# Kernel tuning notes

Hardware: AMD Instinct MI355X
Metric: run time of the kernel (lower is better)

Reference implementation:

```python
import jax, jax.numpy as jnp
import numpy as np

D = 768          # TGLU_hidden_dim == input_hidden_dim
E = 8            # num_experts
TOP_K = 2        # top_experts
N_ENT = 32       # num_entity
B = 16           # batch (mentions)
L = 128          # max_seq_len
EPS = 1e-5


def setup_inputs() -> dict:
    key = jax.random.key(0)
    ks = jax.random.split(key, 16)
    s = 0.02
    return {
        "entity_text_cls": jax.random.normal(ks[0], (N_ENT, D), jnp.float32),
        "entity_text_tokens": jax.random.normal(ks[1], (N_ENT, L, D), jnp.float32),
        "mention_text_cls": jax.random.normal(ks[2], (B, D), jnp.float32),
        "mention_text_tokens": jax.random.normal(ks[3], (B, L, D), jnp.float32),
        # SwitchMoE params: gate + per-expert Linear(dim -> output_dim)
        "gate_w": jax.random.normal(ks[4], (D, E), jnp.float32) * s,
        "gate_b": jnp.zeros((E,), jnp.float32),
        "exp_w": jax.random.normal(ks[5], (E, D, D), jnp.float32) * s,
        "exp_b": jnp.zeros((E, D), jnp.float32),
        # attention projections
        "wq": jax.random.normal(ks[6], (D, D), jnp.float32) * s,
        "bq": jnp.zeros((D,), jnp.float32),
        "wk": jax.random.normal(ks[7], (D, D), jnp.float32) * s,
        "bk": jnp.zeros((D,), jnp.float32),
        "wv": jax.random.normal(ks[8], (D, D), jnp.float32) * s,
        "bv": jnp.zeros((D,), jnp.float32),
        # LayerNorm params
        "ln_w": jnp.ones((D,), jnp.float32),
        "ln_b": jnp.zeros((D,), jnp.float32),
    }


def _switch_moe(x, gate_w, gate_b, exp_w, exp_b):
    # x: [n, s, D] -> [n, s, D]; top-k router, renormalized combine.
    logits = jnp.einsum("nsd,de->nse", x, gate_w) + gate_b
    probs = jax.nn.softmax(logits, axis=-1)
    vals, idx = jax.lax.top_k(probs, TOP_K)              # [n,s,k]
    vals = vals / jnp.sum(vals, axis=-1, keepdims=True)
    # combine weights over all experts (zero for unselected) -> dense mask form
    w = jnp.sum(jax.nn.one_hot(idx, E, dtype=x.dtype) * vals[..., None], axis=-2)  # [n,s,E]
    eo = jnp.einsum("nsd,edo->nseo", x, exp_w) + exp_b   # [n,s,E,D]
    return jnp.einsum("nse,nseo->nso", w, eo)


def _layernorm(x, w, b):
    mu = jnp.mean(x, axis=-1, keepdims=True)
    var = jnp.mean(jnp.square(x - mu), axis=-1, keepdims=True)
    return (x - mu) * jax.lax.rsqrt(var + EPS) * w + b


def reference(entity_text_cls, entity_text_tokens, mention_text_cls, mention_text_tokens,
              gate_w, gate_b, exp_w, exp_b, wq, bq, wk, bk, wv, bv, ln_w, ln_b):
    # prepend CLS, route through shared MoE
    ent = jnp.concatenate([entity_text_cls[:, None, :], entity_text_tokens], axis=1)   # [N,L+1,D]
    ent_moe = _switch_moe(ent, gate_w, gate_b, exp_w, exp_b)
    ent_cls_moe = ent_moe[:, 0, :]          # [N,D]
    ent_tok = ent_moe[:, 1:, :]             # [N,L,D]

    men = jnp.concatenate([mention_text_cls[:, None, :], mention_text_tokens], axis=1)  # [B,L+1,D]
    men_moe = _switch_moe(men, gate_w, gate_b, exp_w, exp_b)
    men_tok = men_moe[:, 1:, :]             # [B,L,D]

    q = jnp.einsum("nld,do->nlo", ent_tok, wq) + bq    # [N,L,D]
    k = jnp.einsum("bmd,do->bmo", men_tok, wk) + bk    # [B,L,D]
    v = jnp.einsum("bmd,do->bmo", men_tok, wv) + bv    # [B,L,D]

    # all-pairs entity x mention cross attention: [N,B,L,L]
    scores = jnp.einsum("nld,bmd->nblm", q, k) / jnp.sqrt(jnp.asarray(D, q.dtype))
    probs = jax.nn.softmax(scores, axis=-1)
    context = jnp.einsum("nblm,bmd->nbld", probs, v)   # [N,B,L,D]
    context = jnp.mean(context, axis=-2)               # [N,B,D]
    context = _layernorm(context, ln_w, ln_b)

    g2l = jnp.sum(ent_cls_moe[:, None, :] * context, axis=-1)   # [N,B]
    g2l = g2l.T                                                  # [B,N]
    g2g = mention_text_cls @ entity_text_cls.T                   # [B,N]
    return (g2l + g2g) / 2
```

## Files before the change

kernel.cpp:

```cpp
#include <hip/hip_runtime.h>
#include <math.h>

#define D 768
#define NE 8
#define NTOK 6192
#define MEN_TOK0 4128

typedef __attribute__((ext_vector_type(8))) short short8;
typedef __attribute__((ext_vector_type(4))) short short4b;
typedef __attribute__((ext_vector_type(4))) float floatx4;

__device__ __forceinline__ short f2bf(float f) {
  union { float f; unsigned u; } x; x.f = f;
  unsigned r = x.u + 0x7fffu + ((x.u >> 16) & 1u);
  return (short)(r >> 16);
}
__device__ __forceinline__ float bf2f(short s) {
  union { unsigned u; float f; } x; x.u = ((unsigned)(unsigned short)s) << 16;
  return x.f;
}

__device__ __forceinline__ void gload16(const short* g, short8* lds_base) {
  __builtin_amdgcn_global_load_lds(
      (const __attribute__((address_space(1))) unsigned int*)g,
      (__attribute__((address_space(3))) unsigned int*)lds_base,
      16, 0, 0);
}

__device__ __forceinline__ const float* token_row(int t,
    const float* __restrict__ ecls, const float* __restrict__ etok,
    const float* __restrict__ mcls, const float* __restrict__ mtok) {
  if (t < MEN_TOK0) {
    int n = t / 129, s = t - n * 129;
    return (s == 0) ? (ecls + n * D) : (etok + (size_t)(n * 128 + s - 1) * D);
  } else {
    int tm = t - MEN_TOK0;
    int b = tm / 129, s = tm - b * 129;
    return (s == 0) ? (mcls + b * D) : (mtok + (size_t)(b * 128 + s - 1) * D);
  }
}

__global__ __launch_bounds__(256) void prep_kernel(
    const float* __restrict__ ecls, const float* __restrict__ etok,
    const float* __restrict__ mcls, const float* __restrict__ mtok,
    const float* __restrict__ gate_w, const float* __restrict__ gate_b,
    const float* __restrict__ exp_w, const float* __restrict__ wq,
    const float* __restrict__ wk, const float* __restrict__ wv,
    int* __restrict__ te1, int* __restrict__ te2,
    float* __restrict__ tw1, float* __restrict__ tw2,
    short* __restrict__ Xb, short* __restrict__ expwT, short* __restrict__ wT) {
  __shared__ float tbuf[64][65];
  int bid = blockIdx.x;
  int tid = threadIdx.x;
  if (bid < 1548) {
    int t = bid * 4 + (tid >> 6);
    int lane = tid & 63;
    const float* xr = token_row(t, ecls, etok, mcls, mtok);
    float acc[NE];
#pragma unroll
    for (int e = 0; e < NE; ++e) acc[e] = 0.f;
#pragma unroll
    for (int it = 0; it < 3; ++it) {
      int d0 = lane * 4 + it * 256;
      floatx4 x = *(const floatx4*)(xr + d0);
      short4b xb;
#pragma unroll
      for (int q = 0; q < 4; ++q) {
        xb[q] = f2bf(x[q]);
        float xv = x[q];
#pragma unroll
        for (int e = 0; e < NE; ++e) acc[e] += xv * gate_w[(d0 + q) * NE + e];
      }
      *(short4b*)(Xb + (size_t)t * D + d0) = xb;
    }
#pragma unroll
    for (int e = 0; e < NE; ++e) {
#pragma unroll
      for (int off = 32; off > 0; off >>= 1) acc[e] += __shfl_down(acc[e], off);
    }
    if (lane == 0) {
      float lg[NE];
#pragma unroll
      for (int e = 0; e < NE; ++e) lg[e] = acc[e] + gate_b[e];
      int e1 = 0;
#pragma unroll
      for (int e = 1; e < NE; ++e) if (lg[e] > lg[e1]) e1 = e;
      int e2 = (e1 == 0) ? 1 : 0;
#pragma unroll
      for (int e = 0; e < NE; ++e) {
        if (e != e1 && lg[e] > lg[e2]) e2 = e;
      }
      float w1 = 1.f / (1.f + __expf(lg[e2] - lg[e1]));
      te1[t] = e1; te2[t] = e2;
      tw1[t] = w1; tw2[t] = 1.f - w1;
    }
  } else {
    int zz = bid - 1548;
    int z = zz / 144, rem = zz % 144;
    int k0 = (rem / 12) * 64, o0 = (rem % 12) * 64;
    const float* src; short* dst;
    if (z < 8) { src = exp_w + (size_t)z * D * D; dst = expwT + (size_t)z * D * D; }
    else { src = (z == 8) ? wq : (z == 9) ? wk : wv; dst = wT + (size_t)(z - 8) * D * D; }
    int tx = tid & 63, ty = tid >> 6;
#pragma unroll
    for (int i = 0; i < 16; ++i) {
      int k = i * 4 + ty;
      tbuf[k][tx] = src[(size_t)(k0 + k) * D + o0 + tx];
    }
    __syncthreads();
#pragma unroll
    for (int i = 0; i < 16; ++i) {
      int o = i * 4 + ty;
      dst[(size_t)(o0 + o) * D + k0 + tx] = f2bf(tbuf[tx][o]);
    }
  }
}

__global__ __launch_bounds__(1024) void route_kernel(
    const int* __restrict__ te1, const int* __restrict__ te2,
    int* __restrict__ lst_tok, int* __restrict__ slot1, int* __restrict__ slot2,
    int* __restrict__ cnt, int* __restrict__ basee) {
  __shared__ int hist[NE];
  __shared__ int base_s[NE];
  int tid = threadIdx.x;
  if (tid < NE) hist[tid] = 0;
  __syncthreads();
  for (int t = tid; t < NTOK; t += 1024) {
    atomicAdd(&hist[te1[t]], 1);
    atomicAdd(&hist[te2[t]], 1);
  }
  __syncthreads();
  if (tid == 0) {
    int acc = 0;
    for (int e = 0; e < NE; ++e) {
      base_s[e] = acc;
      cnt[e] = hist[e];
      basee[e] = acc;
      acc += hist[e];
    }
  }
  __syncthreads();
  if (tid < NE) hist[tid] = 0;
  __syncthreads();
  for (int t = tid; t < NTOK; t += 1024) {
    int e1 = te1[t], e2 = te2[t];
    int r1 = atomicAdd(&hist[e1], 1);
    int r2 = atomicAdd(&hist[e2], 1);
    int s1 = base_s[e1] + r1;
    int s2 = base_s[e2] + r2;
    slot1[t] = s1; slot2[t] = s2;
    lst_tok[s1] = t; lst_tok[s2] = t;
  }
}

__global__ __launch_bounds__(512, 4) void moe_kernel(
    const short* __restrict__ Xb, const short* __restrict__ expwT,
    const int* __restrict__ cnt, const int* __restrict__ basee,
    const int* __restrict__ lst_tok, short* __restrict__ EO) {
  int id = blockIdx.x;
  int e = id & 7;
  int r = id >> 3;
  int ob = r % 6;
  int tb = r / 6;
  int count = cnt[e];
  int t0 = tb * 128;
  if (t0 >= count) return;
  int o0 = ob * 128;
  int gb = basee[e];

  __shared__ short8 As[1024];
  __shared__ short8 Bs[1024];
  __shared__ int stok[128];

  int tid = threadIdx.x;
  int l = tid & 63, w = tid >> 6;
  int wr = w >> 1, wc = w & 1;

  if (tid < 128) {
    int p = t0 + tid;
    stok[tid] = lst_tok[gb + (p < count ? p : 0)];
  }
  __syncthreads();

  const short* Bg = expwT + (size_t)e * D * D;
  int srow = tid >> 2, scc = tid & 3;
  int csrc = (scc ^ ((srow >> 1) & 3)) * 8;
  const short* srcA = Xb + (size_t)stok[srow] * D + csrc;
  const short* srcB = Bg + (size_t)(o0 + srow) * D + csrc;

  floatx4 acc[2][4];
#pragma unroll
  for (int ai = 0; ai < 2; ++ai)
#pragma unroll
    for (int bj = 0; bj < 4; ++bj) acc[ai][bj] = (floatx4){0.f, 0.f, 0.f, 0.f};

  gload16(srcA, &As[w << 6]);
  gload16(srcB, &Bs[w << 6]);
  __syncthreads();

  for (int it = 0; it < 24; ++it) {
    int cur = (it & 1) << 9;
    if (it < 23) {
      int k0n = (it + 1) * 32;
      gload16(srcA + k0n, &As[(cur ^ 512) + (w << 6)]);
      gload16(srcB + k0n, &Bs[(cur ^ 512) + (w << 6)]);
    }
    int kc = l >> 4;
    short8 a[2], bb[4];
#pragma unroll
    for (int ai = 0; ai < 2; ++ai) {
      int ar = wr * 32 + ai * 16 + (l & 15);
      a[ai] = As[cur + (ar << 2) + (kc ^ ((ar >> 1) & 3))];
    }
#pragma unroll
    for (int bj = 0; bj < 4; ++bj) {
      int br = wc * 64 + bj * 16 + (l & 15);
      bb[bj] = Bs[cur + (br << 2) + (kc ^ ((br >> 1) & 3))];
    }
#pragma unroll
    for (int ai = 0; ai < 2; ++ai)
#pragma unroll
      for (int bj = 0; bj < 4; ++bj)
        acc[ai][bj] = __builtin_amdgcn_mfma_f32_16x16x32_bf16(a[ai], bb[bj], acc[ai][bj], 0, 0, 0);
    __syncthreads();
  }

#pragma unroll
  for (int ai = 0; ai < 2; ++ai) {
#pragma unroll
    for (int rr = 0; rr < 4; ++rr) {
      int rowl = wr * 32 + ai * 16 + ((l >> 4) << 2) + rr;
      int p = t0 + rowl;
      if (p < count) {
        size_t off = (size_t)(gb + p) * D;
#pragma unroll
        for (int bj = 0; bj < 4; ++bj) {
          int col = o0 + wc * 64 + bj * 16 + (l & 15);
          EO[off + col] = f2bf(acc[ai][bj][rr]);
        }
      }
    }
  }
}

__global__ __launch_bounds__(256) void combine_kernel(
    const short* __restrict__ EO,
    const int* __restrict__ te1, const int* __restrict__ te2,
    const float* __restrict__ tw1, const float* __restrict__ tw2,
    const int* __restrict__ slot1, const int* __restrict__ slot2,
    const float* __restrict__ exp_b, short* __restrict__ MOEb) {
  int idx = blockIdx.x * 256 + threadIdx.x;
  int t = idx / 96, cg = idx - t * 96;
  int c0 = cg * 8;
  int e1 = te1[t], e2 = te2[t];
  float w1 = tw1[t], w2 = tw2[t];
  short8 a = *(const short8*)(EO + (size_t)slot1[t] * D + c0);
  short8 b = *(const short8*)(EO + (size_t)slot2[t] * D + c0);
  const float* b1 = exp_b + e1 * D + c0;
  const float* b2 = exp_b + e2 * D + c0;
  short8 o;
#pragma unroll
  for (int j = 0; j < 8; ++j)
    o[j] = f2bf(w1 * (bf2f(a[j]) + b1[j]) + w2 * (bf2f(b[j]) + b2[j]));
  *(short8*)(MOEb + (size_t)t * D + c0) = o;
}

__global__ __launch_bounds__(512, 4) void qkv_kernel(
    const short* __restrict__ MOEb, const short* __restrict__ wT,
    const float* __restrict__ bq, const float* __restrict__ bk,
    const float* __restrict__ bv,
    short* __restrict__ Qb, short* __restrict__ Kb, short* __restrict__ Vb) {
  int id = blockIdx.x;
  int z, r;
  if (id < 384)      { z = 0; r = id; }
  else if (id < 576) { z = 1; r = id - 384; }
  else               { z = 2; r = id - 576; }
  int tb = r / 6, ob = r % 6;
  int o0 = ob * 128;
  int base = (z == 0) ? 0 : MEN_TOK0;
  const short* W = wT + (size_t)z * D * D;
  const float* bias = (z == 0) ? bq : (z == 1) ? bk : bv;
  int tokbase = base + (tb >> 1) * 129 + 1 + (tb & 1) * 64;
  const short* Ag = MOEb + (size_t)tokbase * D;

  __shared__ short8 As[512];
  __shared__ short8 Bs[1024];

  int tid = threadIdx.x;
  int l = tid & 63, w = tid >> 6;
  int wr = w >> 1, wc = w & 1;

  int srow = tid >> 2, scc = tid & 3;
  int csrc = (scc ^ ((srow >> 1) & 3)) * 8;
  const short* srcA = Ag + (size_t)(srow & 63) * D + csrc;
  const short* srcB = W + (size_t)(o0 + srow) * D + csrc;

  floatx4 acc[4];
#pragma unroll
  for (int bj = 0; bj < 4; ++bj) acc[bj] = (floatx4){0.f, 0.f, 0.f, 0.f};

  if (w < 4) gload16(srcA, &As[w << 6]);
  gload16(srcB, &Bs[w << 6]);
  __syncthreads();

  for (int it = 0; it < 24; ++it) {
    int curA = (it & 1) << 8;
    int curB = (it & 1) << 9;
    if (it < 23) {
      int k0n = (it + 1) * 32;
      if (w < 4) gload16(srcA + k0n, &As[(curA ^ 256) + (w << 6)]);
      gload16(srcB + k0n, &Bs[(curB ^ 512) + (w << 6)]);
    }
    int kc = l >> 4;
    int ar = wr * 16 + (l & 15);
    short8 a = As[curA + (ar << 2) + (kc ^ ((ar >> 1) & 3))];
    short8 bb[4];
#pragma unroll
    for (int bj = 0; bj < 4; ++bj) {
      int br = wc * 64 + bj * 16 + (l & 15);
      bb[bj] = Bs[curB + (br << 2) + (kc ^ ((br >> 1) & 3))];
    }
#pragma unroll
    for (int bj = 0; bj < 4; ++bj)
      acc[bj] = __builtin_amdgcn_mfma_f32_16x16x32_bf16(a, bb[bj], acc[bj], 0, 0, 0);
    __syncthreads();
  }

#pragma unroll
  for (int rr = 0; rr < 4; ++rr) {
    int rowl = wr * 16 + ((l >> 4) << 2) + rr;
    size_t rglob = (size_t)tb * 64 + rowl;
#pragma unroll
    for (int bj = 0; bj < 4; ++bj) {
      int col = o0 + wc * 64 + bj * 16 + (l & 15);
      float v = acc[bj][rr] + bias[col];
      if (z == 0)      Qb[rglob * D + col] = f2bf(v);
      else if (z == 1) Kb[rglob * D + col] = f2bf(v);
      else             Vb[rglob * D + col] = f2bf(v);
    }
  }
}

__device__ __forceinline__ float blockSum512(float v, volatile float* red, int tid) {
#pragma unroll
  for (int off = 32; off > 0; off >>= 1) v += __shfl_down(v, off);
  __syncthreads();
  if ((tid & 63) == 0) red[tid >> 6] = v;
  __syncthreads();
  float s = 0.f;
#pragma unroll
  for (int i = 0; i < 8; ++i) s += red[i];
  return s;
}

__global__ __launch_bounds__(512, 4) void attn_kernel(
    const short* __restrict__ Qb, const short* __restrict__ Kb,
    const short* __restrict__ Vb, const short* __restrict__ MOEb,
    const float* __restrict__ ecls, const float* __restrict__ mcls,
    const float* __restrict__ ln_w, const float* __restrict__ ln_b,
    float* __restrict__ out) {
  int id = blockIdx.x;
  int n = id & 31, b = id >> 5;
  __shared__ short8 Qs[1024];
  __shared__ short8 Ks[1024];
  __shared__ float pb[128];
  __shared__ float red[8];
  int tid = threadIdx.x;
  int l = tid & 63, w = tid >> 6;
  if (tid < 128) pb[tid] = 0.f;

  floatx4 acc[8];
#pragma unroll
  for (int j = 0; j < 8; ++j) acc[j] = (floatx4){0.f, 0.f, 0.f, 0.f};

  const short* qg = Qb + (size_t)n * 128 * D;
  const short* kg = Kb + (size_t)b * 128 * D;

  int srow = tid >> 2, scc = tid & 3;
  int csrc = (scc ^ ((srow >> 1) & 3)) * 8;
  const short* srcQ = qg + (size_t)srow * D + csrc;
  const short* srcK = kg + (size_t)srow * D + csrc;

  gload16(srcQ, &Qs[w << 6]);
  gload16(srcK, &Ks[w << 6]);
  __syncthreads();

  for (int it = 0; it < 24; ++it) {
    int cur = (it & 1) << 9;
    if (it < 23) {
      int k0n = (it + 1) * 32;
      gload16(srcQ + k0n, &Qs[(cur ^ 512) + (w << 6)]);
      gload16(srcK + k0n, &Ks[(cur ^ 512) + (w << 6)]);
    }
    int kc = l >> 4;
    int ar = w * 16 + (l & 15);
    short8 a = Qs[cur + (ar << 2) + (kc ^ ((ar >> 1) & 3))];
    short8 bb[8];
#pragma unroll
    for (int j = 0; j < 8; ++j) {
      int br = j * 16 + (l & 15);
      bb[j] = Ks[cur + (br << 2) + (kc ^ ((br >> 1) & 3))];
    }
#pragma unroll
    for (int j = 0; j < 8; ++j)
      acc[j] = __builtin_amdgcn_mfma_f32_16x16x32_bf16(a, bb[j], acc[j], 0, 0, 0);
    __syncthreads();
  }

  const float scale = 0.03608439182435161f;
  float colsum[8];
#pragma unroll
  for (int j = 0; j < 8; ++j) colsum[j] = 0.f;

#pragma unroll
  for (int r = 0; r < 4; ++r) {
    float mx = -3.0e38f;
#pragma unroll
    for (int j = 0; j < 8; ++j) mx = fmaxf(mx, acc[j][r]);
    mx = fmaxf(mx, __shfl_xor(mx, 1));
    mx = fmaxf(mx, __shfl_xor(mx, 2));
    mx = fmaxf(mx, __shfl_xor(mx, 4));
    mx = fmaxf(mx, __shfl_xor(mx, 8));
    float pv[8], sm = 0.f;
#pragma unroll
    for (int j = 0; j < 8; ++j) { pv[j] = __expf((acc[j][r] - mx) * scale); sm += pv[j]; }
    sm += __shfl_xor(sm, 1);
    sm += __shfl_xor(sm, 2);
    sm += __shfl_xor(sm, 4);
    sm += __shfl_xor(sm, 8);
    float inv = 1.f / sm;
#pragma unroll
    for (int j = 0; j < 8; ++j) colsum[j] += pv[j] * inv;
  }
#pragma unroll
  for (int j = 0; j < 8; ++j) {
    colsum[j] += __shfl_xor(colsum[j], 16);
    colsum[j] += __shfl_xor(colsum[j], 32);
  }
  if (l < 16) {
#pragma unroll
    for (int j = 0; j < 8; ++j) atomicAdd(&pb[j * 16 + l], colsum[j]);
  }
  __syncthreads();

  int d2 = (tid & 255) + 512;
  float ctx0 = 0.f, ctx1 = 0.f;
  const short* vb = Vb + (size_t)b * 128 * D;
  for (int m = 0; m < 128; ++m) {
    float p = pb[m];
    const short* row = vb + (size_t)m * D;
    ctx0 += p * bf2f(row[tid]);
    ctx1 += p * bf2f(row[d2]);
  }
  ctx0 *= (1.f / 128.f);
  ctx1 *= (1.f / 128.f);
  bool lo = tid < 256;

  float mu = blockSum512(ctx0 + (lo ? ctx1 : 0.f), red, tid) * (1.f / 768.f);
  float c0 = ctx0 - mu, c1 = ctx1 - mu;
  float vs = c0 * c0 + (lo ? c1 * c1 : 0.f);
  float var = blockSum512(vs, red, tid) * (1.f / 768.f);
  float rstd = rsqrtf(var + 1e-5f);

  const short* em = MOEb + (size_t)(n * 129) * D;
  float cl0 = c0 * rstd * ln_w[tid] + ln_b[tid];
  float cl1 = c1 * rstd * ln_w[d2] + ln_b[d2];
  float g2l_p = bf2f(em[tid]) * cl0 + (lo ? bf2f(em[d2]) * cl1 : 0.f);
  float g2g_p = mcls[(size_t)b * D + tid] * ecls[(size_t)n * D + tid] +
                (lo ? mcls[(size_t)b * D + d2] * ecls[(size_t)n * D + d2] : 0.f);
  float g2l = blockSum512(g2l_p, red, tid);
  float g2g = blockSum512(g2g_p, red, tid);
  if (tid == 0) out[b * 32 + n] = 0.5f * (g2l + g2g);
}

extern "C" void kernel_launch(void* const* d_in, const int* in_sizes, int n_in,
                              void* d_out, int out_size, void* d_ws, size_t ws_size,
                              hipStream_t stream) {
  const float* ecls   = (const float*)d_in[0];
  const float* etok   = (const float*)d_in[1];
  const float* mcls   = (const float*)d_in[2];
  const float* mtok   = (const float*)d_in[3];
  const float* gate_w = (const float*)d_in[4];
  const float* gate_b = (const float*)d_in[5];
  const float* exp_w  = (const float*)d_in[6];
  const float* exp_b  = (const float*)d_in[7];
  const float* wq     = (const float*)d_in[8];
  const float* bq     = (const float*)d_in[9];
  const float* wk     = (const float*)d_in[10];
  const float* bk     = (const float*)d_in[11];
  const float* wv     = (const float*)d_in[12];
  const float* bv     = (const float*)d_in[13];
  const float* ln_w   = (const float*)d_in[14];
  const float* ln_b   = (const float*)d_in[15];
  float* outp = (float*)d_out;

  char* ws = (char*)d_ws;
  short* Qb    = (short*)(ws + 0);
  short* Kb    = (short*)(ws + 6291456);
  short* Vb    = (short*)(ws + 9437184);
  short* Xb    = (short*)(ws + 12582912);
  short* EO    = (short*)(ws + 22093824);
  short* MOEb  = (short*)(ws + 41115648);
  short* expwT = (short*)(ws + 50626560);
  short* wT    = (short*)(ws + 60063744);
  int*   te1   = (int*)  (ws + 63602688);
  int*   te2   = (int*)  (ws + 63627456);
  float* tw1   = (float*)(ws + 63652224);
  float* tw2   = (float*)(ws + 63676992);
  int*   slot1 = (int*)  (ws + 63701760);
  int*   slot2 = (int*)  (ws + 63726528);
  int*   lst_tok = (int*)(ws + 63751296);
  int*   cnt   = (int*)  (ws + 63800832);
  int*   basee = (int*)  (ws + 63800864);

  prep_kernel<<<1548 + 1584, 256, 0, stream>>>(ecls, etok, mcls, mtok, gate_w, gate_b,
                                               exp_w, wq, wk, wv,
                                               te1, te2, tw1, tw2, Xb, expwT, wT);
  route_kernel<<<1, 1024, 0, stream>>>(te1, te2, lst_tok, slot1, slot2, cnt, basee);
  moe_kernel<<<49 * 6 * 8, 512, 0, stream>>>(Xb, expwT, cnt, basee, lst_tok, EO);
  combine_kernel<<<2322, 256, 0, stream>>>(EO, te1, te2, tw1, tw2, slot1, slot2,
                                           exp_b, MOEb);
  qkv_kernel<<<768, 512, 0, stream>>>(MOEb, wT, bq, bk, bv, Qb, Kb, Vb);
  attn_kernel<<<512, 512, 0, stream>>>(Qb, Kb, Vb, MOEb, ecls, mcls, ln_w, ln_b, outp);
}
```

Before: 124.9 us.

## Triple-buffer GEMM loads with single barrier per iteration and vectorize attn epilogue

Converts the double-buffered LDS pipelines in the MoE, QKV and attention-score kernels to triple buffering with a prefetch distance of two, using explicit vmcnt waits and one barrier per k-step instead of two syncthreads. This aims to hide global-to-LDS load latency behind MFMA work. The attention epilogue also changes so 192 threads each handle four contiguous columns with vector loads, replacing scalar strided loads. LDS use grows by half, which may lower occupancy, and the hand-tuned vmcnt counts must match the number of loads each wave issues.

Result: faster. 121.3 us (-2.9%).

```diff
diff --git a/kernel.cpp b/kernel.cpp
--- a/kernel.cpp
+++ b/kernel.cpp
@@ -26,6 +26,14 @@
       (__attribute__((address_space(3))) unsigned int*)lds_base,
       16, 0, 0);
 }
+
+#define PIPE_BAR(NSTR)                                            \
+  do {                                                            \
+    asm volatile("s_waitcnt vmcnt(" NSTR ")" ::: "memory");       \
+    __builtin_amdgcn_sched_barrier(0);                            \
+    __builtin_amdgcn_s_barrier();                                 \
+    __builtin_amdgcn_sched_barrier(0);                            \
+  } while (0)
 
 __device__ __forceinline__ const float* token_row(int t,
     const float* __restrict__ ecls, const float* __restrict__ etok,
@@ -168,8 +176,8 @@
   int o0 = ob * 128;
   int gb = basee[e];
 
-  __shared__ short8 As[1024];
-  __shared__ short8 Bs[1024];
+  __shared__ short8 As[1536];
+  __shared__ short8 Bs[1536];
   __shared__ int stok[128];
 
   int tid = threadIdx.x;
@@ -196,14 +204,17 @@
 
   gload16(srcA, &As[w << 6]);
   gload16(srcB, &Bs[w << 6]);
-  __syncthreads();
+  gload16(srcA + 32, &As[512 + (w << 6)]);
+  gload16(srcB + 32, &Bs[512 + (w << 6)]);
 
   for (int it = 0; it < 24; ++it) {
-    int cur = (it & 1) << 9;
-    if (it < 23) {
-      int k0n = (it + 1) * 32;
-      gload16(srcA + k0n, &As[(cur ^ 512) + (w << 6)]);
-      gload16(srcB + k0n, &Bs[(cur ^ 512) + (w << 6)]);
+    if (it < 23) PIPE_BAR("2"); else PIPE_BAR("0");
+    int cur = (it % 3) << 9;
+    if (it < 22) {
+      int nb = ((it + 2) % 3) << 9;
+      int k0n = (it + 2) * 32;
+      gload16(srcA + k0n, &As[nb + (w << 6)]);
+      gload16(srcB + k0n, &Bs[nb + (w << 6)]);
     }
     int kc = l >> 4;
     short8 a[2], bb[4];
@@ -222,7 +233,6 @@
 #pragma unroll
       for (int bj = 0; bj < 4; ++bj)
         acc[ai][bj] = __builtin_amdgcn_mfma_f32_16x16x32_bf16(a[ai], bb[bj], acc[ai][bj], 0, 0, 0);
-    __syncthreads();
   }
 
 #pragma unroll
@@ -283,8 +293,8 @@
   int tokbase = base + (tb >> 1) * 129 + 1 + (tb & 1) * 64;
   const short* Ag = MOEb + (size_t)tokbase * D;
 
-  __shared__ short8 As[512];
-  __shared__ short8 Bs[1024];
+  __shared__ short8 As[768];
+  __shared__ short8 Bs[1536];
 
   int tid = threadIdx.x;
   int l = tid & 63, w = tid >> 6;
@@ -301,15 +311,30 @@
 
   if (w < 4) gload16(srcA, &As[w << 6]);
   gload16(srcB, &Bs[w << 6]);
-  __syncthreads();
+  if (w < 4) gload16(srcA + 32, &As[256 + (w << 6)]);
+  gload16(srcB + 32, &Bs[512 + (w << 6)]);
 
   for (int it = 0; it < 24; ++it) {
-    int curA = (it & 1) << 8;
-    int curB = (it & 1) << 9;
     if (it < 23) {
-      int k0n = (it + 1) * 32;
-      if (w < 4) gload16(srcA + k0n, &As[(curA ^ 256) + (w << 6)]);
-      gload16(srcB + k0n, &Bs[(curB ^ 512) + (w << 6)]);
+      if (w < 4) {
+        asm volatile("s_waitcnt vmcnt(2)" ::: "memory");
+      } else {
+        asm volatile("s_waitcnt vmcnt(1)" ::: "memory");
+      }
+    } else {
+      asm volatile("s_waitcnt vmcnt(0)" ::: "memory");
+    }
+    __builtin_amdgcn_sched_barrier(0);
+    __builtin_amdgcn_s_barrier();
+    __builtin_amdgcn_sched_barrier(0);
+
+    int curA = (it % 3) << 8;
+    int curB = (it % 3) << 9;
+    if (it < 22) {
+      int nb = (it + 2) % 3;
+      int k0n = (it + 2) * 32;
+      if (w < 4) gload16(srcA + k0n, &As[(nb << 8) + (w << 6)]);
+      gload16(srcB + k0n, &Bs[(nb << 9) + (w << 6)]);
     }
     int kc = l >> 4;
     int ar = wr * 16 + (l & 15);
@@ -323,7 +348,6 @@
 #pragma unroll
     for (int bj = 0; bj < 4; ++bj)
       acc[bj] = __builtin_amdgcn_mfma_f32_16x16x32_bf16(a, bb[bj], acc[bj], 0, 0, 0);
-    __syncthreads();
   }
 
 #pragma unroll
@@ -361,13 +385,14 @@
     float* __restrict__ out) {
   int id = blockIdx.x;
   int n = id & 31, b = id >> 5;
-  __shared__ short8 Qs[1024];
-  __shared__ short8 Ks[1024];
+  __shared__ short8 Qs[1536];
+  __shared__ short8 Ks[1536];
   __shared__ float pb[128];
   __shared__ float red[8];
   int tid = threadIdx.x;
   int l = tid & 63, w = tid >> 6;
   if (tid < 128) pb[tid] = 0.f;
+  __syncthreads();
 
   floatx4 acc[8];
 #pragma unroll
@@ -383,14 +408,17 @@
 
   gload16(srcQ, &Qs[w << 6]);
   gload16(srcK, &Ks[w << 6]);
-  __syncthreads();
+  gload16(srcQ + 32, &Qs[512 + (w << 6)]);
+  gload16(srcK + 32, &Ks[512 + (w << 6)]);
 
   for (int it = 0; it < 24; ++it) {
-    int cur = (it & 1) << 9;
-    if (it < 23) {
-      int k0n = (it + 1) * 32;
-      gload16(srcQ + k0n, &Qs[(cur ^ 512) + (w << 6)]);
-      gload16(srcK + k0n, &Ks[(cur ^ 512) + (w << 6)]);
+    if (it < 23) PIPE_BAR("2"); else PIPE_BAR("0");
+    int cur = (it % 3) << 9;
+    if (it < 22) {
+      int nb = ((it + 2) % 3) << 9;
+      int k0n = (it + 2) * 32;
+      gload16(srcQ + k0n, &Qs[nb + (w << 6)]);
+      gload16(srcK + k0n, &Ks[nb + (w << 6)]);
     }
     int kc = l >> 4;
     int ar = w * 16 + (l & 15);
@@ -404,7 +432,6 @@
 #pragma unroll
     for (int j = 0; j < 8; ++j)
       acc[j] = __builtin_amdgcn_mfma_f32_16x16x32_bf16(a, bb[j], acc[j], 0, 0, 0);
-    __syncthreads();
   }
 
   const float scale = 0.03608439182435161f;
@@ -443,31 +470,43 @@
   }
   __syncthreads();
 
-  int d2 = (tid & 255) + 512;
-  float ctx0 = 0.f, ctx1 = 0.f;
-  const short* vb = Vb + (size_t)b * 128 * D;
-  for (int m = 0; m < 128; ++m) {
-    float p = pb[m];
-    const short* row = vb + (size_t)m * D;
-    ctx0 += p * bf2f(row[tid]);
-    ctx1 += p * bf2f(row[d2]);
-  }
-  ctx0 *= (1.f / 128.f);
-  ctx1 *= (1.f / 128.f);
-  bool lo = tid < 256;
-
-  float mu = blockSum512(ctx0 + (lo ? ctx1 : 0.f), red, tid) * (1.f / 768.f);
-  float c0 = ctx0 - mu, c1 = ctx1 - mu;
-  float vs = c0 * c0 + (lo ? c1 * c1 : 0.f);
+  float ctx[4] = {0.f, 0.f, 0.f, 0.f};
+  bool act = tid < 192;
+  int d0 = tid << 2;
+  if (act) {
+    const short* vb = Vb + (size_t)b * 128 * D + d0;
+    for (int m = 0; m < 128; ++m) {
+      float p = pb[m];
+      short4b v = *(const short4b*)(vb + (size_t)m * D);
+#pragma unroll
+      for (int j = 0; j < 4; ++j) ctx[j] += p * bf2f(v[j]);
+    }
+#pragma unroll
+    for (int j = 0; j < 4; ++j) ctx[j] *= (1.f / 128.f);
+  }
+
+  float mu = blockSum512(ctx[0] + ctx[1] + ctx[2] + ctx[3], red, tid) * (1.f / 768.f);
+  float c[4];
+#pragma unroll
+  for (int j = 0; j < 4; ++j) c[j] = ctx[j] - mu;
+  float vs = act ? (c[0]*c[0] + c[1]*c[1] + c[2]*c[2] + c[3]*c[3]) : 0.f;
   float var = blockSum512(vs, red, tid) * (1.f / 768.f);
   float rstd = rsqrtf(var + 1e-5f);
 
-  const short* em = MOEb + (size_t)(n * 129) * D;
-  float cl0 = c0 * rstd * ln_w[tid] + ln_b[tid];
-  float cl1 = c1 * rstd * ln_w[d2] + ln_b[d2];
-  float g2l_p = bf2f(em[tid]) * cl0 + (lo ? bf2f(em[d2]) * cl1 : 0.f);
-  float g2g_p = mcls[(size_t)b * D + tid] * ecls[(size_t)n * D + tid] +
-                (lo ? mcls[(size_t)b * D + d2] * ecls[(size_t)n * D + d2] : 0.f);
+  float g2l_p = 0.f, g2g_p = 0.f;
+  if (act) {
+    floatx4 lw = *(const floatx4*)(ln_w + d0);
+    floatx4 lb = *(const floatx4*)(ln_b + d0);
+    short4b em = *(const short4b*)(MOEb + (size_t)(n * 129) * D + d0);
+    floatx4 mc = *(const floatx4*)(mcls + (size_t)b * D + d0);
+    floatx4 ec = *(const floatx4*)(ecls + (size_t)n * D + d0);
+#pragma unroll
+    for (int j = 0; j < 4; ++j) {
+      float cl = c[j] * rstd * lw[j] + lb[j];
+      g2l_p += bf2f(em[j]) * cl;
+      g2g_p += mc[j] * ec[j];
+    }
+  }
   float g2l = blockSum512(g2l_p, red, tid);
   float g2g = blockSum512(g2g_p, red, tid);
   if (tid == 0) out[b * 32 + n] = 0.5f * (g2l + g2g);
```
